# Kernel tuning notes

Hardware: AMD Instinct MI355X
Metric: run time of the kernel (lower is better)

Reference implementation:

```python
import jax, jax.numpy as jnp
import numpy as np

EPS = 1e-8

def rms_norm(x, scale):
    # full RMSNorm over last dim (p < 0 branch): norm/sqrt(d)
    d = x.shape[-1]
    norm = jnp.linalg.norm(x, ord=2, axis=-1, keepdims=True)
    rms = norm * (d ** -0.5)
    return scale * (x / (rms + EPS))

def setup_inputs() -> dict:
    key = jax.random.key(0)
    ks = jax.random.split(key, 4)
    B, N, C, H = 2, 2048, 1024, 16
    hd = C // H
    x = jax.random.normal(ks[0], (B, N, C), dtype=jnp.float32)
    Wqkv = jax.random.normal(ks[1], (C, 3 * C), dtype=jnp.float32) * (C ** -0.5)
    Wproj = jax.random.normal(ks[2], (C, C), dtype=jnp.float32) * (C ** -0.5)
    bproj = jnp.zeros((C,), dtype=jnp.float32)
    q_scale = jnp.ones((hd,), dtype=jnp.float32)
    k_scale = jnp.ones((hd,), dtype=jnp.float32)
    return {"x": x, "Wqkv": Wqkv, "Wproj": Wproj, "bproj": bproj,
            "q_scale": q_scale, "k_scale": k_scale}

def reference(x, Wqkv, Wproj, bproj, q_scale, k_scale):
    B, N, C = x.shape
    H = 16
    hd = C // H
    scale = hd ** -0.5
    qkv = (x @ Wqkv).reshape(B, N, 3, H, hd)
    qkv = jnp.transpose(qkv, (2, 0, 3, 1, 4))  # t b h n c
    q, k, v = qkv[0], qkv[1], qkv[2]
    q = rms_norm(q, q_scale)
    k = rms_norm(k, k_scale)
    attn = jnp.einsum('bhnc,bhmc->bhnm', q, k) * scale
    attn = jax.nn.softmax(attn, axis=-1)
    out = jnp.einsum('bhnm,bhmc->bhnc', attn, v)
    out = jnp.transpose(out, (0, 2, 1, 3)).reshape(B, N, C)
    return out @ Wproj + bproj
```

## Files before the change

kernel.cpp:

```cpp
#include <hip/hip_runtime.h>


typedef _Float16 half_t;
typedef __attribute__((ext_vector_type(2))) __fp16 fp16x2;
typedef __attribute__((ext_vector_type(4))) _Float16 half4v;
typedef __attribute__((ext_vector_type(8))) _Float16 half8;
typedef __attribute__((ext_vector_type(4))) float f32x4;

#define DI __device__ __forceinline__

DI void gl_lds16(const void* g, void* l) {
    __builtin_amdgcn_global_load_lds((const __attribute__((address_space(1))) void*)g,
                                     (__attribute__((address_space(3))) void*)l, 16, 0, 0);
}

DI float exp2_fast(float x) {
    float r;
    asm("v_exp_f32 %0, %1" : "=v"(r) : "v"(x));
    return r;
}

__global__ void prep_all(const float* __restrict__ x, const float* __restrict__ Wqkv,
                         const float* __restrict__ Wproj, half_t* __restrict__ xh,
                         half_t* __restrict__ wqt, half_t* __restrict__ wpt) {
    __shared__ float t[32][33];
    int bid = blockIdx.x;
    if (bid < 4096) {
        int i = (bid * 256 + threadIdx.x) * 4;
        float4 v = *(const float4*)(x + i);
        half4v o;
        o[0] = (half_t)v.x; o[1] = (half_t)v.y; o[2] = (half_t)v.z; o[3] = (half_t)v.w;
        *(half4v*)(xh + i) = o;
    } else if (bid < 4096 + 3072) {
        int i = bid - 4096;
        int c0 = (i % 96) * 32, r0 = (i / 96) * 32;
        int tx = threadIdx.x & 31, ty = threadIdx.x >> 5;
#pragma unroll
        for (int k = 0; k < 4; k++)
            t[ty + 8 * k][tx] = Wqkv[(size_t)(r0 + ty + 8 * k) * 3072 + c0 + tx];
        __syncthreads();
#pragma unroll
        for (int k = 0; k < 4; k++)
            wqt[(size_t)(c0 + ty + 8 * k) * 1024 + r0 + tx] = (half_t)t[tx][ty + 8 * k];
    } else {
        int i = bid - 4096 - 3072;
        int c0 = (i % 32) * 32, r0 = (i / 32) * 32;
        int tx = threadIdx.x & 31, ty = threadIdx.x >> 5;
#pragma unroll
        for (int k = 0; k < 4; k++)
            t[ty + 8 * k][tx] = Wproj[(size_t)(r0 + ty + 8 * k) * 1024 + c0 + tx];
        __syncthreads();
#pragma unroll
        for (int k = 0; k < 4; k++)
            wpt[(size_t)(c0 + ty + 8 * k) * 1024 + r0 + tx] = (half_t)t[tx][ty + 8 * k];
    }
}

__global__ __launch_bounds__(256) void gemm_qkv(
    const half_t* __restrict__ A, const half_t* __restrict__ Bt,
    const float* __restrict__ qs, const float* __restrict__ ks,
    half_t* __restrict__ qh, half_t* __restrict__ kh, half_t* __restrict__ vth) {
    const int K = 1024;
    __shared__ __align__(16) half_t Al[2][128 * 64];
    __shared__ __align__(16) half_t Bl[2][128 * 64];
    int tid = threadIdx.x;
    int w = tid >> 6, l = tid & 63;
    int wr = w >> 1, wc = w & 1;
    int g = l >> 4, r = l & 15;
    int m0 = blockIdx.x * 128, n0 = blockIdx.y * 128;
    f32x4 acc[4][4] = {};

#define STAGE_QKV(kt, buf)                                                        \
    {                                                                             \
        _Pragma("unroll")                                                         \
        for (int p = 0; p < 4; p++) {                                             \
            int ci = p * 256 + tid;                                               \
            int row = ci >> 3, c = ci & 7, lc = c ^ (row & 7);                    \
            gl_lds16(A + (size_t)(m0 + row) * K + (kt) * 64 + lc * 8,             \
                     &Al[buf][0] + ci * 8);                                       \
            gl_lds16(Bt + (size_t)(n0 + row) * K + (kt) * 64 + lc * 8,            \
                     &Bl[buf][0] + ci * 8);                                       \
        }                                                                         \
    }

    STAGE_QKV(0, 0);
    __syncthreads();
    int cur = 0;
    for (int kt = 0; kt < 16; kt++) {
        if (kt < 15) STAGE_QKV(kt + 1, cur ^ 1);
#pragma unroll
        for (int ks2 = 0; ks2 < 2; ks2++) {
            half8 af[4], bf[4];
#pragma unroll
            for (int i = 0; i < 4; i++) {
                int row = wr * 64 + i * 16 + r;
                af[i] = *(const half8*)(&Al[cur][0] + row * 64 + (((4 * ks2 + g) ^ (row & 7)) << 3));
                int rowb = wc * 64 + i * 16 + r;
                bf[i] = *(const half8*)(&Bl[cur][0] + rowb * 64 + (((4 * ks2 + g) ^ (rowb & 7)) << 3));
            }
#pragma unroll
            for (int i = 0; i < 4; i++)
#pragma unroll
                for (int j = 0; j < 4; j++)
                    acc[i][j] = __builtin_amdgcn_mfma_f32_16x16x32_f16(af[i], bf[j], acc[i][j], 0, 0, 0);
        }
        __syncthreads();
        cur ^= 1;
    }

    int tsec = n0 >> 10;
    if (tsec == 2) {
#pragma unroll
        for (int i = 0; i < 4; i++)
#pragma unroll
            for (int j = 0; j < 4; j++) {
                int gcol = n0 + wc * 64 + j * 16 + r;
                int h = (gcol >> 6) & 15;
                int f = gcol & 63;
                int growb = m0 + wr * 64 + i * 16 + g * 4;
                int b = growb >> 11;
                int n = growb & 2047;
                half4v pv;
#pragma unroll
                for (int rr = 0; rr < 4; rr++) pv[rr] = (half_t)acc[i][j][rr];
                *(half4v*)(vth + ((size_t)(b * 16 + h) * 64 + f) * 2048 + n) = pv;
            }
    } else {
        const float* sc = (tsec == 0) ? qs : ks;
        half_t* dst = (tsec == 0) ? qh : kh;
        float extra = (tsec == 0) ? (0.125f * 1.44269504f) : 1.0f;
        float scv[4];
#pragma unroll
        for (int j = 0; j < 4; j++) scv[j] = sc[j * 16 + r];
#pragma unroll
        for (int i = 0; i < 4; i++)
#pragma unroll
            for (int rr = 0; rr < 4; rr++) {
                float ss = 0.f;
#pragma unroll
                for (int j = 0; j < 4; j++) ss += acc[i][j][rr] * acc[i][j][rr];
#pragma unroll
                for (int d = 1; d < 16; d <<= 1) ss += __shfl_xor(ss, d, 64);
                float inv = extra / (sqrtf(ss) * 0.125f + 1e-8f);
                int grow = m0 + wr * 64 + i * 16 + g * 4 + rr;
                int b = grow >> 11;
                int n = grow & 2047;
#pragma unroll
                for (int j = 0; j < 4; j++) {
                    int gcol = n0 + wc * 64 + j * 16 + r;
                    int h = (gcol >> 6) & 15;
                    int f = gcol & 63;
                    dst[((size_t)(b * 16 + h) * 2048 + n) * 64 + f] =
                        (half_t)(acc[i][j][rr] * inv * scv[j]);
                }
            }
    }
}

__global__ __launch_bounds__(256, 4) void attn(
    const half_t* __restrict__ qh, const half_t* __restrict__ kh,
    const half_t* __restrict__ vth, half_t* __restrict__ aoh) {
    int bh = blockIdx.y;
    int q0 = blockIdx.x * 64;
    const half_t* Qp = qh + (size_t)bh * 2048 * 64;
    const half_t* Kp = kh + (size_t)bh * 2048 * 64;
    const half_t* Vp = vth + (size_t)bh * 64 * 2048;
    __shared__ __align__(16) half_t Kl[2][64 * 64];
    __shared__ __align__(16) half_t Vl[2][64 * 64];
    __shared__ __align__(16) half_t Pl[4][16 * 64];
    int tid = threadIdx.x, w = tid >> 6, l = tid & 63, g = l >> 4, r = l & 15;

    const half_t* kstp[2];
    const half_t* vstp[2];
    int ldsoff[2];
#pragma unroll
    for (int p = 0; p < 2; p++) {
        int ci = p * 256 + tid;
        int row = ci >> 3, c = ci & 7, lc = c ^ (row & 7);
        kstp[p] = Kp + (size_t)row * 64 + lc * 8;
        vstp[p] = Vp + (size_t)row * 2048 + lc * 8;
        ldsoff[p] = ci * 8;
    }

    int koff[8], voff[8], poffw[4], poffr[2];
#pragma unroll
    for (int ks = 0; ks < 2; ks++)
#pragma unroll
        for (int tt = 0; tt < 4; tt++) {
            int row = tt * 16 + r;
            koff[ks * 4 + tt] = row * 64 + (((4 * ks + g) ^ (row & 7)) << 3);
        }
#pragma unroll
    for (int ks2 = 0; ks2 < 2; ks2++)
#pragma unroll
        for (int cf = 0; cf < 4; cf++) {
            int row = cf * 16 + r;
            voff[ks2 * 4 + cf] = row * 64 + (((4 * ks2 + g) ^ (row & 7)) << 3);
        }
#pragma unroll
    for (int tt = 0; tt < 4; tt++)
        poffw[tt] = r * 64 + (((2 * tt + (g >> 1)) ^ (r & 7)) << 3) + (g & 1) * 4;
#pragma unroll
    for (int ks2 = 0; ks2 < 2; ks2++)
        poffr[ks2] = r * 64 + (((4 * ks2 + g) ^ (r & 7)) << 3);
    half_t* Pw = &Pl[w][0];

    half8 qf[2];
#pragma unroll
    for (int ks = 0; ks < 2; ks++)
        qf[ks] = *(const half8*)(Qp + (size_t)(q0 + w * 16 + r) * 64 + ks * 32 + g * 8);

    f32x4 o[4] = {};
    float m = -1e30f, lsum = 0.f;

#pragma unroll
    for (int p = 0; p < 2; p++) {
        gl_lds16(kstp[p], &Kl[0][0] + ldsoff[p]);
        gl_lds16(vstp[p], &Vl[0][0] + ldsoff[p]);
    }
    __syncthreads();

#define ATTN_TILE(BUF, T)                                                          \
    {                                                                              \
        if ((T) < 31) {                                                            \
            _Pragma("unroll")                                                      \
            for (int p = 0; p < 2; p++) {                                          \
                gl_lds16(kstp[p] + ((T) + 1) * 4096, &Kl[(BUF) ^ 1][0] + ldsoff[p]); \
                gl_lds16(vstp[p] + ((T) + 1) * 64, &Vl[(BUF) ^ 1][0] + ldsoff[p]); \
            }                                                                      \
        }                                                                          \
        const half_t* Kc = &Kl[BUF][0];                                            \
        const half_t* Vc = &Vl[BUF][0];                                            \
        f32x4 s[4] = {};                                                           \
        __builtin_amdgcn_s_setprio(1);                                             \
        _Pragma("unroll")                                                          \
        for (int ks = 0; ks < 2; ks++)                                             \
            _Pragma("unroll")                                                      \
            for (int tt = 0; tt < 4; tt++) {                                       \
                half8 kf = *(const half8*)(Kc + koff[ks * 4 + tt]);                \
                s[tt] = __builtin_amdgcn_mfma_f32_16x16x32_f16(kf, qf[ks], s[tt], 0, 0, 0); \
            }                                                                      \
        __builtin_amdgcn_s_setprio(0);                                             \
        float mx = -1e30f;                                                         \
        _Pragma("unroll")                                                          \
        for (int tt = 0; tt < 4; tt++)                                             \
            mx = fmaxf(mx, fmaxf(fmaxf(s[tt][0], s[tt][1]), fmaxf(s[tt][2], s[tt][3]))); \
        mx = fmaxf(mx, __shfl_xor(mx, 16, 64));                                    \
        mx = fmaxf(mx, __shfl_xor(mx, 32, 64));                                    \
        if (!__all(mx <= m + 11.0f)) {                                             \
            float mn = fmaxf(m, mx);                                               \
            float fac = exp2_fast(m - mn);                                         \
            lsum *= fac;                                                           \
            _Pragma("unroll")                                                      \
            for (int cf = 0; cf < 4; cf++) {                                       \
                o[cf][0] *= fac; o[cf][1] *= fac; o[cf][2] *= fac; o[cf][3] *= fac; \
            }                                                                      \
            m = mn;                                                                \
        }                                                                          \
        _Pragma("unroll")                                                          \
        for (int tt = 0; tt < 4; tt++)                                             \
            _Pragma("unroll")                                                      \
            for (int e = 0; e < 4; e++) {                                          \
                float p = exp2_fast(s[tt][e] - m);                                 \
                s[tt][e] = p;                                                      \
                lsum += p;                                                         \
            }                                                                      \
        _Pragma("unroll")                                                          \
        for (int tt = 0; tt < 4; tt++) {                                           \
            fp16x2 a = __builtin_amdgcn_cvt_pkrtz(s[tt][0], s[tt][1]);             \
            fp16x2 b = __builtin_amdgcn_cvt_pkrtz(s[tt][2], s[tt][3]);             \
            half4v v4;                                                             \
            v4[0] = (half_t)a[0]; v4[1] = (half_t)a[1];                            \
            v4[2] = (half_t)b[0]; v4[3] = (half_t)b[1];                            \
            *(half4v*)(Pw + poffw[tt]) = v4;                                       \
        }                                                                          \
        _Pragma("unroll")                                                          \
        for (int ks2 = 0; ks2 < 2; ks2++) {                                        \
            half8 pf = *(const half8*)(Pw + poffr[ks2]);                           \
            __builtin_amdgcn_s_setprio(1);                                         \
            _Pragma("unroll")                                                      \
            for (int cf = 0; cf < 4; cf++) {                                       \
                half8 vf = *(const half8*)(Vc + voff[ks2 * 4 + cf]);               \
                o[cf] = __builtin_amdgcn_mfma_f32_16x16x32_f16(vf, pf, o[cf], 0, 0, 0); \
            }                                                                      \
            __builtin_amdgcn_s_setprio(0);                                         \
        }                                                                          \
        __syncthreads();                                                           \
    }

    for (int t = 0; t < 32; t += 2) {
        ATTN_TILE(0, t);
        ATTN_TILE(1, t + 1);
    }

    lsum += __shfl_xor(lsum, 16, 64);
    lsum += __shfl_xor(lsum, 32, 64);

    int b = bh >> 4, h = bh & 15;
    int n = q0 + w * 16 + r;
    float inv = 1.0f / lsum;
#pragma unroll
    for (int cf = 0; cf < 4; cf++) {
        half4v ov;
#pragma unroll
        for (int reg = 0; reg < 4; reg++) ov[reg] = (half_t)(o[cf][reg] * inv);
        *(half4v*)(aoh + ((size_t)b * 2048 + n) * 1024 + h * 64 + cf * 16 + g * 4) = ov;
    }
}

__global__ __launch_bounds__(256) void gemm_proj(
    const half_t* __restrict__ A, const half_t* __restrict__ Bt,
    const float* __restrict__ bias, float* __restrict__ out) {
    const int K = 1024;
    __shared__ __align__(16) half_t Al[128 * 64];
    __shared__ __align__(16) half_t Bl[128 * 64];
    int tid = threadIdx.x, w = tid >> 6, l = tid & 63;
    int wr = w >> 1, wc = w & 1, g = l >> 4, r = l & 15;
    int m0 = blockIdx.x * 128, n0 = blockIdx.y * 128;
    f32x4 acc[4][4] = {};

    for (int k0 = 0; k0 < K; k0 += 64) {
#pragma unroll
        for (int p = 0; p < 4; p++) {
            int ci = (p * 4 + w) * 64 + l;
            int row = ci >> 3, c = ci & 7;
            int lc = c ^ (row & 7);
            gl_lds16(A + (size_t)(m0 + row) * K + k0 + lc * 8, Al + (p * 4 + w) * 512);
            gl_lds16(Bt + (size_t)(n0 + row) * K + k0 + lc * 8, Bl + (p * 4 + w) * 512);
        }
        __syncthreads();
#pragma unroll
        for (int ks = 0; ks < 2; ks++) {
            half8 af[4], bf[4];
#pragma unroll
            for (int i = 0; i < 4; i++) {
                int row = wr * 64 + i * 16 + r;
                af[i] = *(const half8*)(Al + row * 64 + (((4 * ks + g) ^ (row & 7)) << 3));
                int rowb = wc * 64 + i * 16 + r;
                bf[i] = *(const half8*)(Bl + rowb * 64 + (((4 * ks + g) ^ (rowb & 7)) << 3));
            }
#pragma unroll
            for (int i = 0; i < 4; i++)
#pragma unroll
                for (int j = 0; j < 4; j++)
                    acc[i][j] = __builtin_amdgcn_mfma_f32_16x16x32_f16(af[i], bf[j], acc[i][j], 0, 0, 0);
        }
        __syncthreads();
    }

#pragma unroll
    for (int i = 0; i < 4; i++)
#pragma unroll
        for (int j = 0; j < 4; j++) {
            int gcol = n0 + wc * 64 + j * 16 + r;
            float bv = bias[gcol];
#pragma unroll
            for (int rr = 0; rr < 4; rr++) {
                int grow = m0 + wr * 64 + i * 16 + g * 4 + rr;
                out[(size_t)grow * 1024 + gcol] = acc[i][j][rr] + bv;
            }
        }
}

extern "C" void kernel_launch(void* const* d_in, const int* in_sizes, int n_in,
                              void* d_out, int out_size, void* d_ws, size_t ws_size,
                              hipStream_t stream) {
    const float* x = (const float*)d_in[0];
    const float* Wqkv = (const float*)d_in[1];
    const float* Wproj = (const float*)d_in[2];
    const float* bproj = (const float*)d_in[3];
    const float* qscale = (const float*)d_in[4];
    const float* kscale = (const float*)d_in[5];
    float* out = (float*)d_out;

    char* ws = (char*)d_ws;
    half_t* xh  = (half_t*)(ws + 0);
    half_t* wqt = (half_t*)(ws + 8388608);
    half_t* wpt = (half_t*)(ws + 14680064);
    half_t* qh  = (half_t*)(ws + 16777216);
    half_t* kh  = (half_t*)(ws + 25165824);
    half_t* vth = (half_t*)(ws + 33554432);
    half_t* aoh = (half_t*)(ws + 41943040);

    prep_all<<<8192, 256, 0, stream>>>(x, Wqkv, Wproj, xh, wqt, wpt);
    gemm_qkv<<<dim3(32, 24), 256, 0, stream>>>(xh, wqt, qscale, kscale, qh, kh, vth);
    attn<<<dim3(32, 32), 256, 0, stream>>>(qh, kh, vth, aoh);
    gemm_proj<<<dim3(32, 8), 256, 0, stream>>>(aoh, wpt, bproj, out);
}
```

Baseline: 135.3 us.

## Process two query groups per wave and keep P in registers via permlane swaps

Each attention block now covers 128 queries, so every wave handles two 16-row query groups that share each loaded K/V fragment, halving K/V LDS traffic per query. The P matrix no longer goes through an LDS round trip; it is reshuffled into MFMA operand layout in registers using v_permlane32/16_swap. The rescale check compares elements against the threshold directly before computing the row max. This raises register pressure (launch bounds lowered to 2 blocks per CU) and halves the grid to 512 blocks, which may reduce occupancy and latency hiding.

```diff
diff --git a/kernel.cpp b/kernel.cpp
--- a/kernel.cpp
+++ b/kernel.cpp
@@ -6,6 +6,7 @@
 typedef __attribute__((ext_vector_type(4))) _Float16 half4v;
 typedef __attribute__((ext_vector_type(8))) _Float16 half8;
 typedef __attribute__((ext_vector_type(4))) float f32x4;
+typedef __attribute__((ext_vector_type(4))) unsigned uint4v;
 
 #define DI __device__ __forceinline__
 
@@ -18,6 +19,18 @@
     float r;
     asm("v_exp_f32 %0, %1" : "=v"(r) : "v"(x));
     return r;
+}
+
+DI void pl32_swap(unsigned& a, unsigned& b) {
+    asm("v_permlane32_swap_b32 %0, %1" : "+v"(a), "+v"(b));
+}
+DI void pl16_swap(unsigned& a, unsigned& b) {
+    asm("v_permlane16_swap_b32 %0, %1" : "+v"(a), "+v"(b));
+}
+
+DI unsigned pk_u32(float lo, float hi) {
+    fp16x2 t = __builtin_amdgcn_cvt_pkrtz(lo, hi);
+    return *(unsigned*)&t;
 }
 
 __global__ void prep_all(const float* __restrict__ x, const float* __restrict__ Wqkv,
@@ -157,17 +170,16 @@
     }
 }
 
-__global__ __launch_bounds__(256, 4) void attn(
+__global__ __launch_bounds__(256, 2) void attn(
     const half_t* __restrict__ qh, const half_t* __restrict__ kh,
     const half_t* __restrict__ vth, half_t* __restrict__ aoh) {
     int bh = blockIdx.y;
-    int q0 = blockIdx.x * 64;
+    int q0 = blockIdx.x * 128;
     const half_t* Qp = qh + (size_t)bh * 2048 * 64;
     const half_t* Kp = kh + (size_t)bh * 2048 * 64;
     const half_t* Vp = vth + (size_t)bh * 64 * 2048;
     __shared__ __align__(16) half_t Kl[2][64 * 64];
     __shared__ __align__(16) half_t Vl[2][64 * 64];
-    __shared__ __align__(16) half_t Pl[4][16 * 64];
     int tid = threadIdx.x, w = tid >> 6, l = tid & 63, g = l >> 4, r = l & 15;
 
     const half_t* kstp[2];
@@ -182,7 +194,7 @@
         ldsoff[p] = ci * 8;
     }
 
-    int koff[8], voff[8], poffw[4], poffr[2];
+    int koff[8], voff[8];
 #pragma unroll
     for (int ks = 0; ks < 2; ks++)
 #pragma unroll
@@ -197,21 +209,16 @@
             int row = cf * 16 + r;
             voff[ks2 * 4 + cf] = row * 64 + (((4 * ks2 + g) ^ (row & 7)) << 3);
         }
-#pragma unroll
-    for (int tt = 0; tt < 4; tt++)
-        poffw[tt] = r * 64 + (((2 * tt + (g >> 1)) ^ (r & 7)) << 3) + (g & 1) * 4;
-#pragma unroll
-    for (int ks2 = 0; ks2 < 2; ks2++)
-        poffr[ks2] = r * 64 + (((4 * ks2 + g) ^ (r & 7)) << 3);
-    half_t* Pw = &Pl[w][0];
-
-    half8 qf[2];
-#pragma unroll
-    for (int ks = 0; ks < 2; ks++)
-        qf[ks] = *(const half8*)(Qp + (size_t)(q0 + w * 16 + r) * 64 + ks * 32 + g * 8);
-
-    f32x4 o[4] = {};
-    float m = -1e30f, lsum = 0.f;
+
+    half8 qf[2][2];
+#pragma unroll
+    for (int qg = 0; qg < 2; qg++)
+#pragma unroll
+        for (int ks = 0; ks < 2; ks++)
+            qf[qg][ks] = *(const half8*)(Qp + (size_t)(q0 + w * 32 + qg * 16 + r) * 64 + ks * 32 + g * 8);
+
+    f32x4 o[2][4] = {};
+    float m0v = -1e30f, m1v = -1e30f, ls0 = 0.f, ls1 = 0.f;
 
 #pragma unroll
     for (int p = 0; p < 2; p++) {
@@ -231,59 +238,76 @@
         }                                                                          \
         const half_t* Kc = &Kl[BUF][0];                                            \
         const half_t* Vc = &Vl[BUF][0];                                            \
-        f32x4 s[4] = {};                                                           \
-        __builtin_amdgcn_s_setprio(1);                                             \
+        f32x4 s[2][4] = {};                                                        \
         _Pragma("unroll")                                                          \
         for (int ks = 0; ks < 2; ks++)                                             \
             _Pragma("unroll")                                                      \
             for (int tt = 0; tt < 4; tt++) {                                       \
                 half8 kf = *(const half8*)(Kc + koff[ks * 4 + tt]);                \
-                s[tt] = __builtin_amdgcn_mfma_f32_16x16x32_f16(kf, qf[ks], s[tt], 0, 0, 0); \
+                s[0][tt] = __builtin_amdgcn_mfma_f32_16x16x32_f16(kf, qf[0][ks], s[0][tt], 0, 0, 0); \
+                s[1][tt] = __builtin_amdgcn_mfma_f32_16x16x32_f16(kf, qf[1][ks], s[1][tt], 0, 0, 0); \
             }                                                                      \
-        __builtin_amdgcn_s_setprio(0);                                             \
-        float mx = -1e30f;                                                         \
+        float thr0 = m0v + 11.0f, thr1 = m1v + 11.0f;                              \
+        bool ok = true;                                                            \
         _Pragma("unroll")                                                          \
         for (int tt = 0; tt < 4; tt++)                                             \
-            mx = fmaxf(mx, fmaxf(fmaxf(s[tt][0], s[tt][1]), fmaxf(s[tt][2], s[tt][3]))); \
-        mx = fmaxf(mx, __shfl_xor(mx, 16, 64));                                    \
-        mx = fmaxf(mx, __shfl_xor(mx, 32, 64));                                    \
-        if (!__all(mx <= m + 11.0f)) {                                             \
-            float mn = fmaxf(m, mx);                                               \
-            float fac = exp2_fast(m - mn);                                         \
-            lsum *= fac;                                                           \
-            _Pragma("unroll")                                                      \
-            for (int cf = 0; cf < 4; cf++) {                                       \
-                o[cf][0] *= fac; o[cf][1] *= fac; o[cf][2] *= fac; o[cf][3] *= fac; \
-            }                                                                      \
-            m = mn;                                                                \
+            _Pragma("unroll")                                                      \
+            for (int e = 0; e < 4; e++)                                            \
+                ok = ok && (s[0][tt][e] <= thr0) && (s[1][tt][e] <= thr1);         \
+        if (!__all(ok)) {                                                          \
+            float mx0 = -1e30f, mx1 = -1e30f;                                      \
+            _Pragma("unroll")                                                      \
+            for (int tt = 0; tt < 4; tt++)                                         \
+                _Pragma("unroll")                                                  \
+                for (int e = 0; e < 4; e++) {                                      \
+                    mx0 = fmaxf(mx0, s[0][tt][e]);                                 \
+                    mx1 = fmaxf(mx1, s[1][tt][e]);                                 \
+                }                                                                  \
+            mx0 = fmaxf(mx0, __shfl_xor(mx0, 16, 64));                             \
+            mx0 = fmaxf(mx0, __shfl_xor(mx0, 32, 64));                             \
+            mx1 = fmaxf(mx1, __shfl_xor(mx1, 16, 64));                             \
+            mx1 = fmaxf(mx1, __shfl_xor(mx1, 32, 64));                             \
+            float mn0 = fmaxf(m0v, mx0), mn1 = fmaxf(m1v, mx1);                    \
+            float f0 = exp2_fast(m0v - mn0), f1 = exp2_fast(m1v - mn1);            \
+            ls0 *= f0; ls1 *= f1;                                                  \
+            _Pragma("unroll")                                                      \
+            for (int cf = 0; cf < 4; cf++)                                         \
+                _Pragma("unroll")                                                  \
+                for (int e = 0; e < 4; e++) {                                      \
+                    o[0][cf][e] *= f0;                                             \
+                    o[1][cf][e] *= f1;                                             \
+                }                                                                  \
+            m0v = mn0; m1v = mn1;                                                  \
         }                                                                          \
         _Pragma("unroll")                                                          \
         for (int tt = 0; tt < 4; tt++)                                             \
             _Pragma("unroll")                                                      \
             for (int e = 0; e < 4; e++) {                                          \
-                float p = exp2_fast(s[tt][e] - m);                                 \
-                s[tt][e] = p;                                                      \
-                lsum += p;                                                         \
+                float p0 = exp2_fast(s[0][tt][e] - m0v);                           \
+                float p1 = exp2_fast(s[1][tt][e] - m1v);                           \
+                s[0][tt][e] = p0; ls0 += p0;                                       \
+                s[1][tt][e] = p1; ls1 += p1;                                       \
             }                                                                      \
         _Pragma("unroll")                                                          \
-        for (int tt = 0; tt < 4; tt++) {                                           \
-            fp16x2 a = __builtin_amdgcn_cvt_pkrtz(s[tt][0], s[tt][1]);             \
-            fp16x2 b = __builtin_amdgcn_cvt_pkrtz(s[tt][2], s[tt][3]);             \
-            half4v v4;                                                             \
-            v4[0] = (half_t)a[0]; v4[1] = (half_t)a[1];                            \
-            v4[2] = (half_t)b[0]; v4[3] = (half_t)b[1];                            \
-            *(half4v*)(Pw + poffw[tt]) = v4;                                       \
-        }                                                                          \
-        _Pragma("unroll")                                                          \
         for (int ks2 = 0; ks2 < 2; ks2++) {                                        \
-            half8 pf = *(const half8*)(Pw + poffr[ks2]);                           \
-            __builtin_amdgcn_s_setprio(1);                                         \
+            half8 pf[2];                                                           \
+            _Pragma("unroll")                                                      \
+            for (int qg = 0; qg < 2; qg++) {                                       \
+                unsigned b0 = pk_u32(s[qg][2 * ks2][0], s[qg][2 * ks2][1]);        \
+                unsigned b1 = pk_u32(s[qg][2 * ks2][2], s[qg][2 * ks2][3]);        \
+                unsigned b2 = pk_u32(s[qg][2 * ks2 + 1][0], s[qg][2 * ks2 + 1][1]); \
+                unsigned b3 = pk_u32(s[qg][2 * ks2 + 1][2], s[qg][2 * ks2 + 1][3]); \
+                pl32_swap(b0, b2); pl16_swap(b0, b2);                              \
+                pl32_swap(b1, b3); pl16_swap(b1, b3);                              \
+                uint4v pw; pw[0] = b0; pw[1] = b1; pw[2] = b2; pw[3] = b3;         \
+                pf[qg] = *(half8*)&pw;                                             \
+            }                                                                      \
             _Pragma("unroll")                                                      \
             for (int cf = 0; cf < 4; cf++) {                                       \
                 half8 vf = *(const half8*)(Vc + voff[ks2 * 4 + cf]);               \
-                o[cf] = __builtin_amdgcn_mfma_f32_16x16x32_f16(vf, pf, o[cf], 0, 0, 0); \
+                o[0][cf] = __builtin_amdgcn_mfma_f32_16x16x32_f16(vf, pf[0], o[0][cf], 0, 0, 0); \
+                o[1][cf] = __builtin_amdgcn_mfma_f32_16x16x32_f16(vf, pf[1], o[1][cf], 0, 0, 0); \
             }                                                                      \
-            __builtin_amdgcn_s_setprio(0);                                         \
         }                                                                          \
         __syncthreads();                                                           \
     }
@@ -293,18 +317,23 @@
         ATTN_TILE(1, t + 1);
     }
 
-    lsum += __shfl_xor(lsum, 16, 64);
-    lsum += __shfl_xor(lsum, 32, 64);
+    ls0 += __shfl_xor(ls0, 16, 64);
+    ls0 += __shfl_xor(ls0, 32, 64);
+    ls1 += __shfl_xor(ls1, 16, 64);
+    ls1 += __shfl_xor(ls1, 32, 64);
 
     int b = bh >> 4, h = bh & 15;
-    int n = q0 + w * 16 + r;
-    float inv = 1.0f / lsum;
-#pragma unroll
-    for (int cf = 0; cf < 4; cf++) {
-        half4v ov;
-#pragma unroll
-        for (int reg = 0; reg < 4; reg++) ov[reg] = (half_t)(o[cf][reg] * inv);
-        *(half4v*)(aoh + ((size_t)b * 2048 + n) * 1024 + h * 64 + cf * 16 + g * 4) = ov;
+#pragma unroll
+    for (int qg = 0; qg < 2; qg++) {
+        int n = q0 + w * 32 + qg * 16 + r;
+        float inv = 1.0f / (qg ? ls1 : ls0);
+#pragma unroll
+        for (int cf = 0; cf < 4; cf++) {
+            half4v ov;
+#pragma unroll
+            for (int reg = 0; reg < 4; reg++) ov[reg] = (half_t)(o[qg][cf][reg] * inv);
+            *(half4v*)(aoh + ((size_t)b * 2048 + n) * 1024 + h * 64 + cf * 16 + g * 4) = ov;
+        }
     }
 }
 
@@ -384,6 +413,6 @@
 
     prep_all<<<8192, 256, 0, stream>>>(x, Wqkv, Wproj, xh, wqt, wpt);
     gemm_qkv<<<dim3(32, 24), 256, 0, stream>>>(xh, wqt, qscale, kscale, qh, kh, vth);
-    attn<<<dim3(32, 32), 256, 0, stream>>>(qh, kh, vth, aoh);
+    attn<<<dim3(16, 32), 256, 0, stream>>>(qh, kh, vth, aoh);
     gemm_proj<<<dim3(32, 8), 256, 0, stream>>>(aoh, wpt, bproj, out);
 }
```

New measurement: 132.2 us. 2.3% less time.
